# Kernel optimization log

Hardware: AMD Instinct MI355X
Metric: run time of the kernel (lower is better)

Reference implementation:

```python
import jax, jax.numpy as jnp
import numpy as np

B, DIMS, SIZE = 8, 512, 64
C = DIMS // 2
EPS = 1e-5


def setup_inputs() -> dict:
    key = jax.random.key(0)
    ks = jax.random.split(key, 24)
    f = lambda k, s, sc=0.05: jax.random.normal(k, s, dtype=jnp.float32) * sc
    return {
        "x": jax.random.normal(ks[0], (B, DIMS, SIZE, SIZE), dtype=jnp.float32),
        "cv1_w": f(ks[1], (C, DIMS)),
        "bn1_g": 1.0 + f(ks[2], (C,)),
        "bn1_b": f(ks[3], (C,)),
        "bn1_m": f(ks[4], (C,)),
        "bn1_v": 1.0 + 0.1 * jax.random.uniform(ks[5], (C,), dtype=jnp.float32),
        "q_w": f(ks[6], (C, C)), "q_b": f(ks[7], (C,)),
        "k_w": f(ks[8], (C, C)), "k_b": f(ks[9], (C,)),
        "v_w": f(ks[10], (C, C)), "v_b": f(ks[11], (C,)),
        "e_w": f(ks[12], (C, C)), "e_b": f(ks[13], (C,)),
        "rel_h": f(ks[14], (1, C, SIZE, 1), 1.0) * 0.05,
        "rel_w": f(ks[15], (1, C, 1, SIZE), 1.0) * 0.05,
        "cv2_w": f(ks[16], (DIMS, C)),
        "bn2_g": 1.0 + f(ks[17], (DIMS,)),
        "bn2_b": f(ks[18], (DIMS,)),
        "bn2_m": f(ks[19], (DIMS,)),
        "bn2_v": 1.0 + 0.1 * jax.random.uniform(ks[20], (DIMS,), dtype=jnp.float32),
    }


def _conv1x1(h, w):
    # 1x1 conv == channel contraction
    return jnp.einsum('oc,bchw->bohw', w, h)


def _bn(h, g, b, m, v):
    scale = g / jnp.sqrt(v + EPS)
    return (h - m[None, :, None, None]) * scale[None, :, None, None] + b[None, :, None, None]


def reference(x, cv1_w, bn1_g, bn1_b, bn1_m, bn1_v,
              q_w, q_b, k_w, k_b, v_w, v_b, e_w, e_b,
              rel_h, rel_w, cv2_w, bn2_g, bn2_b, bn2_m, bn2_v):
    x1 = jax.nn.silu(_bn(_conv1x1(x, cv1_w), bn1_g, bn1_b, bn1_m, bn1_v))  # [B,C,H,W]
    Bq, Cc, H, W = x1.shape
    N = H * W

    def proj(w, b):
        return (_conv1x1(x1, w) + b[None, :, None, None]).reshape(Bq, Cc, N)

    q = proj(q_w, q_b)
    k = proj(k_w, k_b)
    v = proj(v_w, v_b)
    e = proj(e_w, e_b)

    # content-content: q^T k  -> [B, N, N]
    cc = jnp.einsum('bcn,bcm->bnm', q, k)
    # content-position: (rel_h + rel_w) broadcast to [C,H,W] -> [C,N]; pos^T @ e
    pos = (rel_h + rel_w).reshape(Cc, N)
    cp = jnp.einsum('cn,bcm->bnm', pos, e)

    attn = jax.nn.softmax(cc + cp, axis=-1)  # [B,N,N]
    # out = v @ attn^T  -> [B,C,N]
    out = jnp.einsum('bcm,bnm->bcn', v, attn).reshape(Bq, Cc, H, W)

    y = jax.nn.silu(_bn(_conv1x1(out, cv2_w), bn2_g, bn2_b, bn2_m, bn2_v))
    return x + y
```

## Files before the change

### kernel.cpp

```cpp
#include <hip/hip_runtime.h>


typedef __bf16 bf16;
typedef __attribute__((ext_vector_type(8))) __bf16 bf16x8;
typedef __attribute__((ext_vector_type(4))) __bf16 bf16x4;
typedef __attribute__((ext_vector_type(2))) __bf16 bf16x2;
typedef __attribute__((ext_vector_type(4))) float f32x4;

__device__ __forceinline__ float silu_f(float x) { return x / (1.f + __expf(-x)); }

__device__ __forceinline__ void zero_acc(f32x4 (&acc)[4][4])
{
#pragma unroll
    for (int i = 0; i < 4; ++i)
#pragma unroll
        for (int j = 0; j < 4; ++j)
            acc[i][j] = (f32x4){0.f, 0.f, 0.f, 0.f};
}

__device__ __forceinline__ void load_lds16(const bf16* g, bf16* l)
{
    __builtin_amdgcn_global_load_lds(
        (const __attribute__((address_space(1))) unsigned int*)g,
        (__attribute__((address_space(3))) unsigned int*)l, 16, 0, 0);
}

__device__ __forceinline__ void wg_barrier()
{
    asm volatile("" ::: "memory");
    __builtin_amdgcn_s_barrier();
    asm volatile("" ::: "memory");
}

__device__ __forceinline__ void gemm_core_db(
    const bf16* __restrict__ A, int lda,
    const bf16* __restrict__ B, int ldb,
    int K, f32x4 (&acc)[4][4])
{
    __shared__ bf16 As[2][128 * 32];
    __shared__ bf16 Bs[2][128 * 32];
    const int tid = threadIdx.x;
    const int wave = tid >> 6;
    const int lane = tid & 63;
    const int lm = lane & 15;
    const int kq = lane >> 4;
    const int m0 = (wave >> 1) * 64;
    const int n0 = (wave & 1) * 64;
    const int srow = tid >> 2;
    const int skoff = (((tid & 3) ^ ((tid >> 3) & 3))) * 8;
    const int krd = (kq ^ ((lm >> 1) & 3)) * 8;
    zero_acc(acc);
    const bf16* ga = A + (size_t)srow * lda + skoff;
    const bf16* gb = B + (size_t)srow * ldb + skoff;
    load_lds16(ga, As[0] + tid * 8);
    load_lds16(ga + (size_t)64 * lda, As[0] + tid * 8 + 64 * 32);
    load_lds16(gb, Bs[0] + tid * 8);
    load_lds16(gb + (size_t)64 * ldb, Bs[0] + tid * 8 + 64 * 32);
    const int nt = K >> 5;
    for (int t = 0; t < nt; ++t) {
        const int cur = t & 1;
        if (t + 1 < nt) {
            const bf16* na = ga + (t + 1) * 32;
            const bf16* nb = gb + (t + 1) * 32;
            bf16* dA = As[cur ^ 1] + tid * 8;
            bf16* dB = Bs[cur ^ 1] + tid * 8;
            load_lds16(na, dA);
            load_lds16(na + (size_t)64 * lda, dA + 64 * 32);
            load_lds16(nb, dB);
            load_lds16(nb + (size_t)64 * ldb, dB + 64 * 32);
            asm volatile("s_waitcnt vmcnt(4)" ::: "memory");
        } else {
            asm volatile("s_waitcnt vmcnt(0)" ::: "memory");
        }
        wg_barrier();
        const bf16* as = As[cur];
        const bf16* bs = Bs[cur];
        bf16x8 av[4], bv[4];
#pragma unroll
        for (int tt = 0; tt < 4; ++tt)
            av[tt] = *(const bf16x8*)(as + (m0 + tt * 16 + lm) * 32 + krd);
#pragma unroll
        for (int tt = 0; tt < 4; ++tt)
            bv[tt] = *(const bf16x8*)(bs + (n0 + tt * 16 + lm) * 32 + krd);
#pragma unroll
        for (int i = 0; i < 4; ++i)
#pragma unroll
            for (int j = 0; j < 4; ++j)
                acc[i][j] = __builtin_amdgcn_mfma_f32_16x16x32_bf16(
                    av[i], bv[j], acc[i][j], 0, 0, 0);
        wg_barrier();
    }
}

__device__ __forceinline__ void gemm_core_256(
    const bf16* __restrict__ A, int lda,
    const bf16* __restrict__ B, int ldb,
    int K, f32x4 (&acc)[8][4])
{
    __shared__ bf16 As[2][16384];
    __shared__ bf16 Bs[2][16384];
    const int tid = threadIdx.x;
    const int lane = tid & 63;
    const int wid = tid >> 6;
    const int wm = wid >> 2, wn = wid & 3;
    const int lm = lane & 15, kq = lane >> 4;
    const int srow = tid >> 3;
    const int skoff = ((tid & 7) ^ (srow & 7)) * 8;
    const bf16* ga = A + (size_t)srow * lda + skoff;
    const bf16* gb = B + (size_t)srow * ldb + skoff;
#pragma unroll
    for (int r = 0; r < 4; ++r)
        load_lds16(ga + (size_t)(64 * r) * lda, As[0] + tid * 8 + r * 4096);
#pragma unroll
    for (int r = 0; r < 4; ++r)
        load_lds16(gb + (size_t)(64 * r) * ldb, Bs[0] + tid * 8 + r * 4096);
#pragma unroll
    for (int i = 0; i < 8; ++i)
#pragma unroll
        for (int j = 0; j < 4; ++j)
            acc[i][j] = (f32x4){0.f, 0.f, 0.f, 0.f};
    const int nt = K >> 6;
    for (int t = 0; t < nt; ++t) {
        const int cur = t & 1;
        if (t + 1 < nt) {
            const bf16* na = ga + (t + 1) * 64;
            const bf16* nb = gb + (t + 1) * 64;
#pragma unroll
            for (int r = 0; r < 4; ++r)
                load_lds16(na + (size_t)(64 * r) * lda,
                           As[cur ^ 1] + tid * 8 + r * 4096);
#pragma unroll
            for (int r = 0; r < 4; ++r)
                load_lds16(nb + (size_t)(64 * r) * ldb,
                           Bs[cur ^ 1] + tid * 8 + r * 4096);
            asm volatile("s_waitcnt vmcnt(8)" ::: "memory");
        } else {
            asm volatile("s_waitcnt vmcnt(0)" ::: "memory");
        }
        wg_barrier();
        const bf16* as = As[cur];
        const bf16* bs = Bs[cur];
#pragma unroll
        for (int ks = 0; ks < 2; ++ks) {
            bf16x8 av[8], bv[4];
#pragma unroll
            for (int i = 0; i < 8; ++i) {
                int lr = wm * 128 + i * 16 + lm;
                av[i] = *(const bf16x8*)(as + lr * 64 +
                                         (((ks << 2) | kq) ^ (lr & 7)) * 8);
            }
#pragma unroll
            for (int j = 0; j < 4; ++j) {
                int lr = wn * 64 + j * 16 + lm;
                bv[j] = *(const bf16x8*)(bs + lr * 64 +
                                         (((ks << 2) | kq) ^ (lr & 7)) * 8);
            }
#pragma unroll
            for (int i = 0; i < 8; ++i)
#pragma unroll
                for (int j = 0; j < 4; ++j)
                    acc[i][j] = __builtin_amdgcn_mfma_f32_16x16x32_bf16(
                        av[i], bv[j], acc[i][j], 0, 0, 0);
        }
        wg_barrier();
    }
}


__global__ __launch_bounds__(256) void prep_misc_kernel(
    const float* __restrict__ cv1_w,
    const float* __restrict__ qw, const float* __restrict__ qb,
    const float* __restrict__ kw, const float* __restrict__ kb,
    const float* __restrict__ vw, const float* __restrict__ vb,
    const float* __restrict__ ew, const float* __restrict__ eb,
    const float* __restrict__ cv2_w,
    const float* __restrict__ g1, const float* __restrict__ b1,
    const float* __restrict__ m1, const float* __restrict__ v1,
    const float* __restrict__ g2, const float* __restrict__ b2,
    const float* __restrict__ m2, const float* __restrict__ v2,
    const float* __restrict__ rel_h, const float* __restrict__ rel_w,
    bf16* __restrict__ w1b, bf16* __restrict__ wqkve, bf16* __restrict__ w2b,
    bf16* __restrict__ posT,
    float* __restrict__ biasq,
    float* __restrict__ bn1s, float* __restrict__ bn1h,
    float* __restrict__ bn2s, float* __restrict__ bn2h)
{
    int idx = blockIdx.x * 256 + threadIdx.x;
    if (idx < 131072) { w1b[idx] = (bf16)cv1_w[idx]; return; }
    idx -= 131072;
    if (idx < 262144) {
        int j = idx >> 8, c = idx & 255;
        int p = j >> 8, r = j & 255;
        const float* w = (p == 0) ? qw : (p == 1) ? kw : (p == 2) ? vw : ew;
        wqkve[idx] = (bf16)w[r * 256 + c];
        return;
    }
    idx -= 262144;
    if (idx < 131072) { w2b[idx] = (bf16)cv2_w[idx]; return; }
    idx -= 131072;
    if (idx < 1024) {
        int p = idx >> 8, r = idx & 255;
        const float* bb = (p == 0) ? qb : (p == 1) ? kb : (p == 2) ? vb : eb;
        biasq[idx] = bb[r];
        return;
    }
    idx -= 1024;
    if (idx < 256) {
        float s = g1[idx] * rsqrtf(v1[idx] + 1e-5f);
        bn1s[idx] = s;
        bn1h[idx] = b1[idx] - m1[idx] * s;
        return;
    }
    idx -= 256;
    if (idx < 512) {
        float s = g2[idx] * rsqrtf(v2[idx] + 1e-5f);
        bn2s[idx] = s;
        bn2h[idx] = b2[idx] - m2[idx] * s;
        return;
    }
    idx -= 512;
    if (idx < 32768) {
        int r = idx >> 8, c = idx & 255;
        posT[idx] = (bf16)((r < 64) ? rel_h[c * 64 + r] : rel_w[c * 64 + (r - 64)]);
        return;
    }
}

__global__ __launch_bounds__(256) void zero_lsum_kernel(float* __restrict__ p)
{
    p[blockIdx.x * 256 + threadIdx.x] = 0.f;
}

__global__ __launch_bounds__(256) void transpose_x_kernel(
    const float* __restrict__ x, bf16* __restrict__ xt)
{
    __shared__ float tile[64][65];
    int b = blockIdx.z;
    int n0 = blockIdx.x * 64;
    int d0 = blockIdx.y * 64;
    int tx = threadIdx.x & 63, ty = threadIdx.x >> 6;
#pragma unroll
    for (int i = 0; i < 16; ++i) {
        int d = i * 4 + ty;
        tile[d][tx] = x[((size_t)(b * 512 + d0 + d)) * 4096 + n0 + tx];
    }
    __syncthreads();
#pragma unroll
    for (int i = 0; i < 16; ++i) {
        int n = i * 4 + ty;
        xt[((size_t)(b * 4096 + n0 + n)) * 512 + d0 + tx] = (bf16)tile[tx][n];
    }
}

__global__ __launch_bounds__(256) void transpose_v_kernel(
    const bf16* __restrict__ v_nm, bf16* __restrict__ v_cm)
{
    __shared__ float tile[64][65];
    int b = blockIdx.z;
    int m0 = blockIdx.x * 64;
    int c0 = blockIdx.y * 64;
    int tx = threadIdx.x & 63, ty = threadIdx.x >> 6;
#pragma unroll
    for (int i = 0; i < 16; ++i) {
        int m = i * 4 + ty;
        tile[m][tx] = (float)v_nm[((size_t)(b * 4096 + m0 + m)) * 256 + c0 + tx];
    }
    __syncthreads();
#pragma unroll
    for (int i = 0; i < 16; ++i) {
        int c = i * 4 + ty;
        v_cm[((size_t)(b * 256 + c0 + c)) * 4096 + m0 + tx] = (bf16)tile[tx][c];
    }
}


__global__ __launch_bounds__(256) void gemm1_kernel(
    const bf16* __restrict__ xt, const bf16* __restrict__ w1b,
    const float* __restrict__ bn1s, const float* __restrict__ bn1h,
    bf16* __restrict__ x1t)
{
    const bf16* A = xt + (size_t)(blockIdx.y * 128) * 512;
    const bf16* Bm = w1b + (size_t)(blockIdx.x * 128) * 512;
    f32x4 acc[4][4];
    gemm_core_db(A, 512, Bm, 512, 512, acc);
    int wave = threadIdx.x >> 6;
    int lane = threadIdx.x & 63;
    int m0 = blockIdx.y * 128 + (wave >> 1) * 64;
    int n0 = blockIdx.x * 128 + (wave & 1) * 64;
    int lm = lane & 15, kq = lane >> 4;
#pragma unroll
    for (int i = 0; i < 4; ++i)
#pragma unroll
        for (int j = 0; j < 4; ++j)
#pragma unroll
            for (int r = 0; r < 4; ++r) {
                int row = m0 + i * 16 + kq * 4 + r;
                int col = n0 + j * 16 + lm;
                float h = bn1s[col] * acc[i][j][r] + bn1h[col];
                x1t[(size_t)row * 256 + col] = (bf16)silu_f(h);
            }
}

__global__ __launch_bounds__(512, 1) void gemm2_kernel(
    const bf16* __restrict__ x1t, const bf16* __restrict__ wqkve,
    const float* __restrict__ biasq,
    bf16* __restrict__ qk, bf16* __restrict__ v_nm, bf16* __restrict__ e_nm)
{
    const int bx = blockIdx.x, by = blockIdx.y;
    const bf16* A = x1t + (size_t)(by * 256) * 256;
    const bf16* Bm = wqkve + (size_t)(bx * 256) * 256;
    f32x4 acc[8][4];
    gemm_core_256(A, 256, Bm, 256, 256, acc);
    const int tid = threadIdx.x, lane = tid & 63, wid = tid >> 6;
    const int wm = wid >> 2, wn = wid & 3, lm = lane & 15, kq = lane >> 4;
#pragma unroll
    for (int i = 0; i < 8; ++i)
#pragma unroll
        for (int j = 0; j < 4; ++j)
#pragma unroll
            for (int r = 0; r < 4; ++r) {
                int row = by * 256 + wm * 128 + i * 16 + kq * 4 + r;
                int col = bx * 256 + wn * 64 + j * 16 + lm;
                bf16 val = (bf16)(acc[i][j][r] + biasq[col]);
                if (bx < 2)          qk[(size_t)row * 512 + col] = val;
                else if (bx == 2)    v_nm[(size_t)row * 256 + (col - 512)] = val;
                else                 e_nm[(size_t)row * 256 + (col - 768)] = val;
            }
}

__global__ __launch_bounds__(256) void gemm_rhw_kernel(
    const bf16* __restrict__ posT, const bf16* __restrict__ e_nm,
    bf16* __restrict__ rhwT)
{
    int b = blockIdx.z;
    const bf16* A = e_nm + ((size_t)b * 4096 + blockIdx.x * 128) * 256;
    f32x4 acc[4][4];
    gemm_core_db(A, 256, posT, 256, 256, acc);
    int wave = threadIdx.x >> 6;
    int lane = threadIdx.x & 63;
    int m0 = (wave >> 1) * 64, n0 = (wave & 1) * 64;
    int lm = lane & 15, kq = lane >> 4;
    bf16* rb = rhwT + ((size_t)b * 4096 + blockIdx.x * 128) * 128;
#pragma unroll
    for (int i = 0; i < 4; ++i)
#pragma unroll
        for (int j = 0; j < 4; ++j)
#pragma unroll
            for (int r = 0; r < 4; ++r)
                rb[(size_t)(m0 + i * 16 + kq * 4 + r) * 128 + n0 + j * 16 + lm] =
                    (bf16)acc[i][j][r];
}

__global__ __launch_bounds__(512, 1) void gemm3b_kernel(
    const bf16* __restrict__ qk, const bf16* __restrict__ rhwT,
    bf16* __restrict__ P, float* __restrict__ lsum, int gbase)
{
    __shared__ float rs[256];
    int flat = blockIdx.x + 16 * blockIdx.y + 256 * blockIdx.z;
    flat = (flat & 7) * 128 + (flat >> 3);
    const int bx = flat & 15, by = (flat >> 4) & 15, bz = flat >> 8;
    const int b = gbase + bz;
    const int tid = threadIdx.x;
    const int wid = tid >> 6;
    const int lane = tid & 63;
    const int wm = wid >> 2, wn = wid & 3;
    const int lm = lane & 15, kq = lane >> 4;
    const bf16* A = qk + ((size_t)b * 4096 + by * 256) * 512;
    const bf16* Bm = qk + ((size_t)b * 4096 + bx * 256) * 512 + 256;
    f32x4 acc[8][4];
    gemm_core_256(A, 512, Bm, 512, 256, acc);
    bf16x2 rhv2[4];
    bf16x4 rwv[4][4];
    {
        const bf16* rbT = rhwT + ((size_t)b * 4096 + bx * 256) * 128;
#pragma unroll
        for (int j = 0; j < 4; ++j) {
            const bf16* cp = rbT + (size_t)(wn * 64 + j * 16 + lm) * 128;
            rhv2[j] = *(const bf16x2*)(cp + by * 4 + wm * 2);
#pragma unroll
            for (int ii = 0; ii < 4; ++ii)
                rwv[j][ii] = *(const bf16x4*)(cp + 64 + ii * 16 + kq * 4);
        }
    }
    if (tid < 256) rs[tid] = 0.f;
    __syncthreads();
    float ps[8][4];
#pragma unroll
    for (int i = 0; i < 8; ++i)
#pragma unroll
        for (int r = 0; r < 4; ++r) {
            float s = 0.f;
#pragma unroll
            for (int j = 0; j < 4; ++j) {
                float sv = acc[i][j][r] + (float)rhv2[j][i >> 2]
                                        + (float)rwv[j][i & 3][r];
                float e = __expf(sv - 8.f);
                acc[i][j][r] = e;
                s += e;
            }
            ps[i][r] = s;
        }
#pragma unroll
    for (int msk = 1; msk < 16; msk <<= 1)
#pragma unroll
        for (int i = 0; i < 8; ++i)
#pragma unroll
            for (int r = 0; r < 4; ++r)
                ps[i][r] += __shfl_xor(ps[i][r], msk);
    if (lm == 0) {
#pragma unroll
        for (int i = 0; i < 8; ++i)
#pragma unroll
            for (int r = 0; r < 4; ++r)
                atomicAdd(&rs[wm * 128 + i * 16 + kq * 4 + r], ps[i][r]);
    }
    bf16* Pb = P + ((size_t)bz * 4096 + by * 256) * 4096 + bx * 256;
#pragma unroll
    for (int i = 0; i < 8; ++i)
#pragma unroll
        for (int j = 0; j < 4; ++j)
#pragma unroll
            for (int r = 0; r < 4; ++r)
                Pb[(size_t)(wm * 128 + i * 16 + kq * 4 + r) * 4096
                   + wn * 64 + j * 16 + lm] = (bf16)acc[i][j][r];
    __syncthreads();
    if (tid < 256)
        atomicAdd(&lsum[(size_t)bz * 4096 + by * 256 + tid], rs[tid]);
}

__global__ __launch_bounds__(512, 1) void gemm4b_kernel(
    const bf16* __restrict__ P, const bf16* __restrict__ v_cm,
    bf16* __restrict__ pacc, int gbase)
{
    int flat = blockIdx.x + 16 * blockIdx.y + 64 * blockIdx.z;
    flat = (flat & 7) * 32 + (flat >> 3);
    const int by = flat & 15, kc = (flat >> 4) & 3, bz = flat >> 6;
    const int b = gbase + bz;
    const bf16* A = P + ((size_t)bz * 4096 + by * 256) * 4096 + kc * 1024;
    const bf16* Bm = v_cm + (size_t)b * 256 * 4096 + kc * 1024;
    f32x4 acc[8][4];
    gemm_core_256(A, 4096, Bm, 4096, 1024, acc);
    const int tid = threadIdx.x, lane = tid & 63, wid = tid >> 6;
    const int wm = wid >> 2, wn = wid & 3, lm = lane & 15, kq = lane >> 4;
    bf16* ob = pacc + ((size_t)kc * 16384 + bz * 4096 + by * 256) * 256;
#pragma unroll
    for (int i = 0; i < 8; ++i)
#pragma unroll
        for (int r = 0; r < 4; ++r)
#pragma unroll
            for (int j = 0; j < 4; ++j)
                ob[(size_t)(wm * 128 + i * 16 + kq * 4 + r) * 256
                   + wn * 64 + j * 16 + lm] = (bf16)acc[i][j][r];
}

__global__ __launch_bounds__(256) void reduce4_kernel(
    const bf16* __restrict__ pacc, const float* __restrict__ lsum,
    bf16* __restrict__ out_t, int gbase)
{
    int t = blockIdx.x * 256 + threadIdx.x;
    int row = t >> 5;
    int c0 = (t & 31) * 8;
    bf16x8 p0 = *(const bf16x8*)(pacc + (size_t)row * 256 + c0);
    bf16x8 p1 = *(const bf16x8*)(pacc + (size_t)(16384 + row) * 256 + c0);
    bf16x8 p2 = *(const bf16x8*)(pacc + (size_t)(32768 + row) * 256 + c0);
    bf16x8 p3 = *(const bf16x8*)(pacc + (size_t)(49152 + row) * 256 + c0);
    float inv = 1.f / lsum[row];
    bf16x8 o;
#pragma unroll
    for (int e = 0; e < 8; ++e)
        o[e] = (bf16)((((float)p0[e] + (float)p1[e]) +
                       ((float)p2[e] + (float)p3[e])) * inv);
    *(bf16x8*)(out_t + ((size_t)gbase * 4096 + row) * 256 + c0) = o;
}

__global__ __launch_bounds__(512, 1) void gemm5_kernel(
    const bf16* __restrict__ w2b, const bf16* __restrict__ out_t,
    const float* __restrict__ bn2s, const float* __restrict__ bn2h,
    const float* __restrict__ x, float* __restrict__ out)
{
    int b = blockIdx.z;
    const bf16* A = w2b + (size_t)(blockIdx.y * 256) * 256;
    const bf16* Bm = out_t + ((size_t)b * 4096 + blockIdx.x * 256) * 256;
    f32x4 acc[8][4];
    gemm_core_256(A, 256, Bm, 256, 256, acc);
    const int tid = threadIdx.x, lane = tid & 63, wid = tid >> 6;
    const int wm = wid >> 2, wn = wid & 3, lm = lane & 15, kq = lane >> 4;
#pragma unroll
    for (int i = 0; i < 8; ++i)
#pragma unroll
        for (int j = 0; j < 4; ++j)
#pragma unroll
            for (int r = 0; r < 4; ++r) {
                int d = blockIdx.y * 256 + wm * 128 + i * 16 + kq * 4 + r;
                int n = blockIdx.x * 256 + wn * 64 + j * 16 + lm;
                float h = bn2s[d] * acc[i][j][r] + bn2h[d];
                size_t gi = ((size_t)(b * 512 + d)) * 4096 + n;
                out[gi] = x[gi] + silu_f(h);
            }
}


extern "C" void kernel_launch(void* const* d_in, const int* in_sizes, int n_in,
                              void* d_out, int out_size, void* d_ws, size_t ws_size,
                              hipStream_t stream)
{
    (void)in_sizes; (void)n_in; (void)out_size; (void)ws_size;
    const float* x     = (const float*)d_in[0];
    const float* cv1_w = (const float*)d_in[1];
    const float* bn1_g = (const float*)d_in[2];
    const float* bn1_b = (const float*)d_in[3];
    const float* bn1_m = (const float*)d_in[4];
    const float* bn1_v = (const float*)d_in[5];
    const float* q_w   = (const float*)d_in[6];
    const float* q_b   = (const float*)d_in[7];
    const float* k_w   = (const float*)d_in[8];
    const float* k_b   = (const float*)d_in[9];
    const float* v_w   = (const float*)d_in[10];
    const float* v_b   = (const float*)d_in[11];
    const float* e_w   = (const float*)d_in[12];
    const float* e_b   = (const float*)d_in[13];
    const float* rel_h = (const float*)d_in[14];
    const float* rel_w = (const float*)d_in[15];
    const float* cv2_w = (const float*)d_in[16];
    const float* bn2_g = (const float*)d_in[17];
    const float* bn2_b = (const float*)d_in[18];
    const float* bn2_m = (const float*)d_in[19];
    const float* bn2_v = (const float*)d_in[20];
    float* out = (float*)d_out;

    char* ws = (char*)d_ws;
    bf16* P     = (bf16*)(ws + 0);
    bf16* xt    = (bf16*)(ws + 0);
    bf16* x1t   = (bf16*)(ws + 33554432);
    bf16* v_nm  = (bf16*)(ws + 50331648);
    bf16* e_nm  = (bf16*)(ws + 67108864);
    bf16* qk    = (bf16*)(ws + 134217728);
    bf16* v_cm  = (bf16*)(ws + 167772160);
    bf16* rhwT  = (bf16*)(ws + 184549376);
    bf16* out_t = (bf16*)(ws + 192937984);
    bf16* w1b   = (bf16*)(ws + 209715200);
    bf16* wqkve = (bf16*)(ws + 209977344);
    bf16* w2b   = (bf16*)(ws + 210501632);
    bf16* posT  = (bf16*)(ws + 210763776);
    float* biasq= (float*)(ws + 210829312);
    float* bn1s = (float*)(ws + 210833408);
    float* bn1h = (float*)(ws + 210834432);
    float* bn2s = (float*)(ws + 210835456);
    float* bn2h = (float*)(ws + 210837504);
    float* lsum = (float*)(ws + 210839552);
    bf16* pacc  = (bf16*)d_out;

    prep_misc_kernel<<<2183, 256, 0, stream>>>(
        cv1_w, q_w, q_b, k_w, k_b, v_w, v_b, e_w, e_b, cv2_w,
        bn1_g, bn1_b, bn1_m, bn1_v, bn2_g, bn2_b, bn2_m, bn2_v,
        rel_h, rel_w,
        w1b, wqkve, w2b, posT, biasq, bn1s, bn1h, bn2s, bn2h);
    zero_lsum_kernel<<<128, 256, 0, stream>>>(lsum);
    transpose_x_kernel<<<dim3(64, 8, 8), 256, 0, stream>>>(x, xt);
    gemm1_kernel<<<dim3(2, 256), 256, 0, stream>>>(xt, w1b, bn1s, bn1h, x1t);
    gemm2_kernel<<<dim3(4, 128), 512, 0, stream>>>(x1t, wqkve, biasq, qk, v_nm, e_nm);
    gemm_rhw_kernel<<<dim3(32, 1, 8), 256, 0, stream>>>(posT, e_nm, rhwT);
    transpose_v_kernel<<<dim3(64, 4, 8), 256, 0, stream>>>(v_nm, v_cm);
    for (int g = 0; g < 2; ++g) {
        float* ls = lsum + (size_t)g * 4 * 4096;
        gemm3b_kernel<<<dim3(16, 16, 4), 512, 0, stream>>>(qk, rhwT, P, ls, g * 4);
        gemm4b_kernel<<<dim3(16, 4, 4), 512, 0, stream>>>(P, v_cm, pacc, g * 4);
        reduce4_kernel<<<2048, 256, 0, stream>>>(pacc, ls, out_t, g * 4);
    }
    gemm5_kernel<<<dim3(16, 2, 8), 512, 0, stream>>>(w2b, out_t, bn2s, bn2h, x, out);
}
```

Baseline: 535.4 us.

## Interleave prefetch with split MFMA phases and raise wave priority in GEMM core

Restructures the shared 256x256 GEMM main loop into four sub-phases, each with its own LDS fragment loads and MFMA batch. The A-tile prefetch is issued before the first phase and the B-tile prefetch after it, spreading global-to-LDS traffic across the compute. s_setprio is raised around the MFMA bursts to favour math waves, and LDS buffers are now declared per kernel and passed in. The extra barriers per K-step add sync overhead, and the early B-buffer write relies on barrier ordering being correct.

```diff
diff --git a/kernel.cpp b/kernel.cpp
--- a/kernel.cpp
+++ b/kernel.cpp
@@ -95,10 +95,8 @@
 __device__ __forceinline__ void gemm_core_256(
     const bf16* __restrict__ A, int lda,
     const bf16* __restrict__ B, int ldb,
-    int K, f32x4 (&acc)[8][4])
-{
-    __shared__ bf16 As[2][16384];
-    __shared__ bf16 Bs[2][16384];
+    int K, f32x4 (&acc)[8][4], bf16* As, bf16* Bs)
+{
     const int tid = threadIdx.x;
     const int lane = tid & 63;
     const int wid = tid >> 6;
@@ -106,14 +104,16 @@
     const int lm = lane & 15, kq = lane >> 4;
     const int srow = tid >> 3;
     const int skoff = ((tid & 7) ^ (srow & 7)) * 8;
+    const int arow = wm * 128 + lm;
+    const int brow = wn * 64 + lm;
     const bf16* ga = A + (size_t)srow * lda + skoff;
     const bf16* gb = B + (size_t)srow * ldb + skoff;
 #pragma unroll
     for (int r = 0; r < 4; ++r)
-        load_lds16(ga + (size_t)(64 * r) * lda, As[0] + tid * 8 + r * 4096);
+        load_lds16(ga + (size_t)(64 * r) * lda, As + tid * 8 + r * 4096);
 #pragma unroll
     for (int r = 0; r < 4; ++r)
-        load_lds16(gb + (size_t)(64 * r) * ldb, Bs[0] + tid * 8 + r * 4096);
+        load_lds16(gb + (size_t)(64 * r) * ldb, Bs + tid * 8 + r * 4096);
 #pragma unroll
     for (int i = 0; i < 8; ++i)
 #pragma unroll
@@ -122,46 +122,93 @@
     const int nt = K >> 6;
     for (int t = 0; t < nt; ++t) {
         const int cur = t & 1;
-        if (t + 1 < nt) {
-            const bf16* na = ga + (t + 1) * 64;
-            const bf16* nb = gb + (t + 1) * 64;
+        const bf16* as = As + cur * 16384;
+        const bf16* bs = Bs + cur * 16384;
+        bf16* dA = As + (cur ^ 1) * 16384;
+        bf16* dB = Bs + (cur ^ 1) * 16384;
+        const bf16* na = ga + (size_t)(t + 1) * 64;
+        const bf16* nb = gb + (size_t)(t + 1) * 64;
+        const bool pf = (t + 1 < nt);
+        bf16x8 av[4], bv[4];
+        if (pf) {
 #pragma unroll
             for (int r = 0; r < 4; ++r)
-                load_lds16(na + (size_t)(64 * r) * lda,
-                           As[cur ^ 1] + tid * 8 + r * 4096);
-#pragma unroll
-            for (int r = 0; r < 4; ++r)
-                load_lds16(nb + (size_t)(64 * r) * ldb,
-                           Bs[cur ^ 1] + tid * 8 + r * 4096);
-            asm volatile("s_waitcnt vmcnt(8)" ::: "memory");
+                load_lds16(na + (size_t)(64 * r) * lda, dA + tid * 8 + r * 4096);
+            asm volatile("s_waitcnt vmcnt(4)" ::: "memory");
         } else {
             asm volatile("s_waitcnt vmcnt(0)" ::: "memory");
         }
         wg_barrier();
-        const bf16* as = As[cur];
-        const bf16* bs = Bs[cur];
-#pragma unroll
-        for (int ks = 0; ks < 2; ++ks) {
-            bf16x8 av[8], bv[4];
-#pragma unroll
-            for (int i = 0; i < 8; ++i) {
-                int lr = wm * 128 + i * 16 + lm;
-                av[i] = *(const bf16x8*)(as + lr * 64 +
-                                         (((ks << 2) | kq) ^ (lr & 7)) * 8);
-            }
-#pragma unroll
-            for (int j = 0; j < 4; ++j) {
-                int lr = wn * 64 + j * 16 + lm;
-                bv[j] = *(const bf16x8*)(bs + lr * 64 +
-                                         (((ks << 2) | kq) ^ (lr & 7)) * 8);
-            }
-#pragma unroll
-            for (int i = 0; i < 8; ++i)
-#pragma unroll
-                for (int j = 0; j < 4; ++j)
-                    acc[i][j] = __builtin_amdgcn_mfma_f32_16x16x32_bf16(
-                        av[i], bv[j], acc[i][j], 0, 0, 0);
-        }
+#pragma unroll
+        for (int j = 0; j < 4; ++j) {
+            int lr = brow + j * 16;
+            bv[j] = *(const bf16x8*)(bs + lr * 64 + (kq ^ (lr & 7)) * 8);
+        }
+#pragma unroll
+        for (int i = 0; i < 4; ++i) {
+            int lr = arow + i * 16;
+            av[i] = *(const bf16x8*)(as + lr * 64 + (kq ^ (lr & 7)) * 8);
+        }
+        __builtin_amdgcn_s_setprio(1);
+#pragma unroll
+        for (int i = 0; i < 4; ++i)
+#pragma unroll
+            for (int j = 0; j < 4; ++j)
+                acc[i][j] = __builtin_amdgcn_mfma_f32_16x16x32_bf16(
+                    av[i], bv[j], acc[i][j], 0, 0, 0);
+        __builtin_amdgcn_s_setprio(0);
+        wg_barrier();
+        if (pf) {
+#pragma unroll
+            for (int r = 0; r < 4; ++r)
+                load_lds16(nb + (size_t)(64 * r) * ldb, dB + tid * 8 + r * 4096);
+        }
+#pragma unroll
+        for (int i = 0; i < 4; ++i) {
+            int lr = arow + (i + 4) * 16;
+            av[i] = *(const bf16x8*)(as + lr * 64 + (kq ^ (lr & 7)) * 8);
+        }
+        __builtin_amdgcn_s_setprio(1);
+#pragma unroll
+        for (int i = 0; i < 4; ++i)
+#pragma unroll
+            for (int j = 0; j < 4; ++j)
+                acc[i + 4][j] = __builtin_amdgcn_mfma_f32_16x16x32_bf16(
+                    av[i], bv[j], acc[i + 4][j], 0, 0, 0);
+        __builtin_amdgcn_s_setprio(0);
+        wg_barrier();
+#pragma unroll
+        for (int j = 0; j < 4; ++j) {
+            int lr = brow + j * 16;
+            bv[j] = *(const bf16x8*)(bs + lr * 64 + ((4 | kq) ^ (lr & 7)) * 8);
+        }
+#pragma unroll
+        for (int i = 0; i < 4; ++i) {
+            int lr = arow + i * 16;
+            av[i] = *(const bf16x8*)(as + lr * 64 + ((4 | kq) ^ (lr & 7)) * 8);
+        }
+        __builtin_amdgcn_s_setprio(1);
+#pragma unroll
+        for (int i = 0; i < 4; ++i)
+#pragma unroll
+            for (int j = 0; j < 4; ++j)
+                acc[i][j] = __builtin_amdgcn_mfma_f32_16x16x32_bf16(
+                    av[i], bv[j], acc[i][j], 0, 0, 0);
+        __builtin_amdgcn_s_setprio(0);
+        wg_barrier();
+#pragma unroll
+        for (int i = 0; i < 4; ++i) {
+            int lr = arow + (i + 4) * 16;
+            av[i] = *(const bf16x8*)(as + lr * 64 + ((4 | kq) ^ (lr & 7)) * 8);
+        }
+        __builtin_amdgcn_s_setprio(1);
+#pragma unroll
+        for (int i = 0; i < 4; ++i)
+#pragma unroll
+            for (int j = 0; j < 4; ++j)
+                acc[i + 4][j] = __builtin_amdgcn_mfma_f32_16x16x32_bf16(
+                    av[i], bv[j], acc[i + 4][j], 0, 0, 0);
+        __builtin_amdgcn_s_setprio(0);
         wg_barrier();
     }
 }
@@ -306,11 +353,12 @@
     const float* __restrict__ biasq,
     bf16* __restrict__ qk, bf16* __restrict__ v_nm, bf16* __restrict__ e_nm)
 {
+    __shared__ bf16 smem[65536];
     const int bx = blockIdx.x, by = blockIdx.y;
     const bf16* A = x1t + (size_t)(by * 256) * 256;
     const bf16* Bm = wqkve + (size_t)(bx * 256) * 256;
     f32x4 acc[8][4];
-    gemm_core_256(A, 256, Bm, 256, 256, acc);
+    gemm_core_256(A, 256, Bm, 256, 256, acc, smem, smem + 32768);
     const int tid = threadIdx.x, lane = tid & 63, wid = tid >> 6;
     const int wm = wid >> 2, wn = wid & 3, lm = lane & 15, kq = lane >> 4;
 #pragma unroll
@@ -355,6 +403,7 @@
     const bf16* __restrict__ qk, const bf16* __restrict__ rhwT,
     bf16* __restrict__ P, float* __restrict__ lsum, int gbase)
 {
+    __shared__ bf16 smem[65536];
     __shared__ float rs[256];
     int flat = blockIdx.x + 16 * blockIdx.y + 256 * blockIdx.z;
     flat = (flat & 7) * 128 + (flat >> 3);
@@ -368,7 +417,7 @@
     const bf16* A = qk + ((size_t)b * 4096 + by * 256) * 512;
     const bf16* Bm = qk + ((size_t)b * 4096 + bx * 256) * 512 + 256;
     f32x4 acc[8][4];
-    gemm_core_256(A, 512, Bm, 512, 256, acc);
+    gemm_core_256(A, 512, Bm, 512, 256, acc, smem, smem + 32768);
     bf16x2 rhv2[4];
     bf16x4 rwv[4][4];
     {
@@ -432,6 +481,7 @@
     const bf16* __restrict__ P, const bf16* __restrict__ v_cm,
     bf16* __restrict__ pacc, int gbase)
 {
+    __shared__ bf16 smem[65536];
     int flat = blockIdx.x + 16 * blockIdx.y + 64 * blockIdx.z;
     flat = (flat & 7) * 32 + (flat >> 3);
     const int by = flat & 15, kc = (flat >> 4) & 3, bz = flat >> 6;
@@ -439,7 +489,7 @@
     const bf16* A = P + ((size_t)bz * 4096 + by * 256) * 4096 + kc * 1024;
     const bf16* Bm = v_cm + (size_t)b * 256 * 4096 + kc * 1024;
     f32x4 acc[8][4];
-    gemm_core_256(A, 4096, Bm, 4096, 1024, acc);
+    gemm_core_256(A, 4096, Bm, 4096, 1024, acc, smem, smem + 32768);
     const int tid = threadIdx.x, lane = tid & 63, wid = tid >> 6;
     const int wm = wid >> 2, wn = wid & 3, lm = lane & 15, kq = lane >> 4;
     bf16* ob = pacc + ((size_t)kc * 16384 + bz * 4096 + by * 256) * 256;
@@ -478,11 +528,12 @@
     const float* __restrict__ bn2s, const float* __restrict__ bn2h,
     const float* __restrict__ x, float* __restrict__ out)
 {
+    __shared__ bf16 smem[65536];
     int b = blockIdx.z;
     const bf16* A = w2b + (size_t)(blockIdx.y * 256) * 256;
     const bf16* Bm = out_t + ((size_t)b * 4096 + blockIdx.x * 256) * 256;
     f32x4 acc[8][4];
-    gemm_core_256(A, 256, Bm, 256, 256, acc);
+    gemm_core_256(A, 256, Bm, 256, 256, acc, smem, smem + 32768);
     const int tid = threadIdx.x, lane = tid & 63, wid = tid >> 6;
     const int wm = wid >> 2, wn = wid & 3, lm = lane & 15, kq = lane >> 4;
 #pragma unroll
```

Measured after the change: 542.6 us. No clear change (+1.3%).
